# Kernel optimization log

Measured on AMD Instinct MI355X. Metric: run time of the kernel, lower is better.

## Reference

```python
import jax, jax.numpy as jnp
import numpy as np

NUM_RELATIONS = 65
NUM_GRAPHS = 1600


def rgcn_conv(x, src, dst, etype, W, Wroot, b):
    """PyG RGCNConv: per-relation mean aggregation + root transform + bias.
    out_i = x_i @ Wroot + b + sum_r mean_{j in N_r(i)} (x_j) @ W_r
    (mean-then-transform == transform-then-mean since W_r is linear).
    """
    N = x.shape[0]
    x_src = x[src]  # [E, in]
    etype_f = etype

    def body(acc, rW):
        r, Wr = rW
        m = (etype_f == r).astype(x.dtype)[:, None]  # [E,1]
        s = jax.ops.segment_sum(x_src * m, dst, num_segments=N)   # [N,in]
        cnt = jax.ops.segment_sum(m, dst, num_segments=N)          # [N,1]
        mean = s / jnp.maximum(cnt, 1.0)
        return acc + mean @ Wr, None

    acc0 = x @ Wroot + b
    out, _ = jax.lax.scan(body, acc0, (jnp.arange(W.shape[0]), W))
    return out


def setup_inputs() -> dict:
    key = jax.random.key(0)
    ks = jax.random.split(key, 20)
    N, E, F, H, M = 50000, 200000, 128, 256, 64
    x = jax.random.normal(ks[0], (N, F), dtype=jnp.float32)
    edge_index = jax.random.randint(ks[1], (2, E), 0, N, dtype=jnp.int64)
    edge_type = jax.random.randint(ks[2], (E,), 0, NUM_RELATIONS, dtype=jnp.int64)
    batch = jnp.sort(jax.random.randint(ks[3], (N,), 0, NUM_GRAPHS, dtype=jnp.int64))

    def glorot(k, shape):
        fan_in = shape[-2] if len(shape) > 1 else shape[-1]
        return jax.random.normal(k, shape, dtype=jnp.float32) / np.sqrt(fan_in)

    W1 = glorot(ks[4], (NUM_RELATIONS, F, H))
    root1 = glorot(ks[5], (F, H))
    b1 = jnp.zeros((H,), jnp.float32)
    W2 = glorot(ks[6], (NUM_RELATIONS, H, H))
    root2 = glorot(ks[7], (H, H))
    b2 = jnp.zeros((H,), jnp.float32)
    ws_w = glorot(ks[8], (H, 1))
    ws_b = jnp.zeros((1,), jnp.float32)
    m1w = glorot(ks[9], (H, M)); m1b = jnp.zeros((M,), jnp.float32)
    m2w = glorot(ks[10], (M, M)); m2b = jnp.zeros((M,), jnp.float32)
    m3w = glorot(ks[11], (M, M)); m3b = jnp.zeros((M,), jnp.float32)
    ow = glorot(ks[12], (M, 1)); ob = jnp.zeros((1,), jnp.float32)
    return {"x": x, "edge_index": edge_index, "edge_type": edge_type, "batch": batch,
            "W1": W1, "root1": root1, "b1": b1, "W2": W2, "root2": root2, "b2": b2,
            "ws_w": ws_w, "ws_b": ws_b, "m1w": m1w, "m1b": m1b, "m2w": m2w,
            "m2b": m2b, "m3w": m3w, "m3b": m3b, "ow": ow, "ob": ob}


def reference(x, edge_index, edge_type, batch, W1, root1, b1, W2, root2, b2,
              ws_w, ws_b, m1w, m1b, m2w, m2b, m3w, m3b, ow, ob):
    N = x.shape[0]
    # add_self_loops(fill_value=0): append self edges with relation 0
    loop = jnp.arange(N, dtype=edge_index.dtype)
    src = jnp.concatenate([edge_index[0], loop])
    dst = jnp.concatenate([edge_index[1], loop])
    et = jnp.concatenate([edge_type, jnp.zeros((N,), edge_type.dtype)])

    h = jax.nn.relu(rgcn_conv(x, src, dst, et, W1, root1, b1))   # dropout: eval
    h = jax.nn.relu(rgcn_conv(h, src, dst, et, W2, root2, b2))

    # WeightedSum pooling
    w = jax.nn.sigmoid(h @ ws_w + ws_b)                          # [N,1]
    emb = jax.ops.segment_sum(w * h, batch, num_segments=NUM_GRAPHS)  # [G,H]

    # MLP (3 layers; eval batch-norm with default stats ~ identity)
    z = jax.nn.relu(emb @ m1w + m1b)
    z = jax.nn.relu(z @ m2w + m2b)
    z = z @ m3w + m3b
    return z @ ow + ob
```

## Files before the change

### kernel.cpp

```cpp
#include <hip/hip_runtime.h>
#include <math.h>

#define N_NODES 50000
#define E_REAL  200000
#define E_MEAN  250000
#define NREL    65
#define HDIM    256
#define NGRAPH  1600
#define NB_R    ((E_REAL + 255) / 256)
#define NB_CNT  ((E_MEAN + 255) / 256)
#define TOT_HIST (NREL * NB_R)
#define MB      64
#define MAX_PB  3264
#define GRID_I  ((N_NODES + MB - 1) / MB)

typedef __attribute__((ext_vector_type(8))) short short8;
typedef __attribute__((ext_vector_type(4))) float floatx4;
typedef const __attribute__((address_space(1))) void GPtr;
typedef __attribute__((address_space(3))) void LPtr;

__device__ __forceinline__ unsigned short f2bf(float f) {
    unsigned int u = __float_as_uint(f);
    unsigned int r = u + 0x7FFFu + ((u >> 16) & 1u);
    return (unsigned short)(r >> 16);
}
__device__ __forceinline__ float bf2f(unsigned short u) {
    return __uint_as_float(((unsigned int)u) << 16);
}

__device__ __forceinline__ void gl_lds16(const unsigned short* g, unsigned short* l) {
    __builtin_amdgcn_global_load_lds((GPtr*)g,
        (LPtr*)(unsigned int)(unsigned long long)(void*)l, 16, 0, 0);
}

__global__ void count_kernel(const int* __restrict__ src, const int* __restrict__ dst,
                             const int* __restrict__ et, int* __restrict__ cnt,
                             int* __restrict__ blockHist, int* __restrict__ cntD) {
    __shared__ int lhist[NREL];
    int t = threadIdx.x;
    if (t < NREL) lhist[t] = 0;
    __syncthreads();
    int e = blockIdx.x * 256 + t;
    if (e < E_REAL) {
        int d = dst[e], r = et[e];
        atomicAdd(&cnt[d * NREL + r], 1);
        atomicAdd(&cntD[d], 1);
        atomicAdd(&lhist[r], 1);
    } else if (e < E_MEAN) {
        atomicAdd(&cnt[(e - E_REAL) * NREL], 1);
    }
    __syncthreads();
    if (t < NREL && blockIdx.x < NB_R) blockHist[t * NB_R + blockIdx.x] = lhist[t];
}

__global__ void scan_part(const int* __restrict__ in, int* __restrict__ psum, int n) {
    __shared__ int red[1024];
    int t = threadIdx.x;
    int g = blockIdx.x * 1024 + t;
    red[t] = (g < n) ? in[g] : 0;
    __syncthreads();
    for (int off = 512; off >= 1; off >>= 1) {
        if (t < off) red[t] += red[t + off];
        __syncthreads();
    }
    if (t == 0) psum[blockIdx.x] = red[0];
}

__global__ void scan_apply(const int* __restrict__ in, const int* __restrict__ psum,
                           int* __restrict__ out, int* __restrict__ out2, int n) {
    __shared__ int sums[1024];
    __shared__ int soff;
    int t = threadIdx.x;
    int b = blockIdx.x;
    int g = b * 1024 + t;
    if (t < 64) {
        int v = (t < b) ? psum[t] : 0;
        for (int off = 32; off >= 1; off >>= 1) v += __shfl_down(v, off, 64);
        if (t == 0) soff = v;
    }
    int v = (g < n) ? in[g] : 0;
    sums[t] = v;
    __syncthreads();
    for (int off = 1; off < 1024; off <<= 1) {
        int u = (t >= off) ? sums[t - off] : 0;
        __syncthreads();
        sums[t] += u;
        __syncthreads();
    }
    if (g < n) {
        int excl = soff + sums[t] - v;
        out[g] = excl;
        if (out2) out2[g] = excl;
    }
}

__global__ void meta_kernel(const int* __restrict__ baseArr,
                            int* __restrict__ relStart, int* __restrict__ relTot,
                            int* __restrict__ pBlockStart, int* __restrict__ relOfBlock,
                            int* __restrict__ npb) {
    __shared__ int sStart[NREL + 1];
    __shared__ int sPB[NREL + 1];
    int t = threadIdx.x;
    if (t < NREL) sStart[t] = baseArr[t * NB_R];
    if (t == 0) sStart[NREL] = E_REAL;
    __syncthreads();
    if (t < NREL) {
        relStart[t] = sStart[t];
        relTot[t] = sStart[t + 1] - sStart[t];
    }
    if (t == 0) {
        int a2 = 0;
        for (int r = 0; r < NREL; ++r) {
            sPB[r] = a2;
            int tot = sStart[r + 1] - sStart[r];
            a2 += (tot + MB - 1) / MB;
        }
        sPB[NREL] = a2;
        npb[0] = a2;
    }
    __syncthreads();
    if (t < NREL) pBlockStart[t] = sPB[t];
    int NPB = sPB[NREL];
    for (int b = t; b < NPB; b += 1024) {
        int lo = 0, hi = NREL - 1;
        while (lo < hi) { int mid = (lo + hi + 1) >> 1; if (sPB[mid] <= b) lo = mid; else hi = mid - 1; }
        relOfBlock[b] = lo;
    }
}

__global__ void scatter_sorted(const int* __restrict__ src, const int* __restrict__ dst,
                               const int* __restrict__ et, const int* __restrict__ base,
                               int* __restrict__ perm, int* __restrict__ cursorD,
                               int* __restrict__ qofp) {
    __shared__ int lhist[NREL];
    int t = threadIdx.x;
    int b = blockIdx.x;
    if (t < NREL) lhist[t] = 0;
    __syncthreads();
    int e = b * 256 + t;
    if (e < E_REAL) {
        int d = dst[e], r = et[e];
        int local = atomicAdd(&lhist[r], 1);
        int p = base[r * NB_R + b] + local;
        perm[p] = e;
        int q = atomicAdd(&cursorD[d], 1);
        qofp[p] = q;
    }
}

__device__ __forceinline__ void cvt_row_chunk(const float* __restrict__ in,
                                              unsigned short* __restrict__ out,
                                              int i, int relu) {
    const float4* p = (const float4*)in + (size_t)i * 2;
    float4 a = p[0], b = p[1];
    float v[8] = {a.x, a.y, a.z, a.w, b.x, b.y, b.z, b.w};
    short8 o;
#pragma unroll
    for (int j = 0; j < 8; ++j) {
        float f = relu ? fmaxf(v[j], 0.f) : v[j];
        o[j] = (short)f2bf(f);
    }
    ((short8*)out)[i] = o;
}
__device__ __forceinline__ void cvt_wT_chunk(const float* __restrict__ W,
                                             unsigned short* __restrict__ out,
                                             int i, int K, int N) {
    int kc8 = K / 8;
    int kc = i % kc8;
    int tmp = i / kc8;
    int n = tmp % N;
    int r = tmp / N;
    const float* src = W + ((size_t)r * K + kc * 8) * N + n;
    short8 o;
#pragma unroll
    for (int j = 0; j < 8; ++j) o[j] = (short)f2bf(src[(size_t)j * N]);
    ((short8*)out)[i] = o;
}

__global__ void cvt_rows(const float* __restrict__ in, unsigned short* __restrict__ out,
                         int nchunk, int relu) {
    int i = blockIdx.x * 256 + threadIdx.x;
    if (i >= nchunk) return;
    cvt_row_chunk(in, out, i, relu);
}

#define CVT_NX  (N_NODES * 128 / 8)
#define CVT_W1  (NREL * 256 * 16)
#define CVT_W2  (NREL * 256 * 32)
#define CVT_R1  (256 * 16)
#define CVT_R2  (256 * 32)
#define CVT_TOT (CVT_NX + CVT_W1 + CVT_W2 + CVT_R1 + CVT_R2)
__global__ void cvt_all(const float* __restrict__ x, const float* __restrict__ W1,
                        const float* __restrict__ W2, const float* __restrict__ root1,
                        const float* __restrict__ root2,
                        unsigned short* __restrict__ xb, unsigned short* __restrict__ w1b,
                        unsigned short* __restrict__ w2b, unsigned short* __restrict__ r1b,
                        unsigned short* __restrict__ r2b) {
    int i = blockIdx.x * 256 + threadIdx.x;
    if (i < CVT_NX) { cvt_row_chunk(x, xb, i, 0); return; }
    i -= CVT_NX;
    if (i < CVT_W1) { cvt_wT_chunk(W1, w1b, i, 128, 256); return; }
    i -= CVT_W1;
    if (i < CVT_W2) { cvt_wT_chunk(W2, w2b, i, 256, 256); return; }
    i -= CVT_W2;
    if (i < CVT_R1) { cvt_wT_chunk(root1, r1b, i, 128, 256); return; }
    i -= CVT_R1;
    if (i < CVT_R2) { cvt_wT_chunk(root2, r2b, i, 256, 256); return; }
}

template<int K>
__device__ __forceinline__ void gemm_pass(const unsigned short* __restrict__ Bp,
                                          const unsigned short* lds,
                                          int lrow, int lk, floatx4 (&acc)[4][4]) {
    constexpr int KS = K / 32;
    short8 bb[3][4];
#pragma unroll
    for (int nf = 0; nf < 4; ++nf)
        bb[0][nf] = *(const short8*)(Bp + (size_t)(nf * 16 + lrow) * K + lk * 8);
#pragma unroll
    for (int nf = 0; nf < 4; ++nf)
        bb[1][nf] = *(const short8*)(Bp + (size_t)(nf * 16 + lrow) * K + 32 + lk * 8);
#pragma unroll
    for (int ks = 0; ks < KS; ++ks) {
        short8 a[4];
#pragma unroll
        for (int mf = 0; mf < 4; ++mf) {
            int row = mf * 16 + lrow;
            int c = (ks * 4 + lk) ^ (row & 7);
            a[mf] = *(const short8*)((const char*)lds + row * (K * 2) + c * 16);
        }
        if (ks + 2 < KS) {
#pragma unroll
            for (int nf = 0; nf < 4; ++nf)
                bb[(ks + 2) % 3][nf] = *(const short8*)(Bp + (size_t)(nf * 16 + lrow) * K + (ks + 2) * 32 + lk * 8);
        }
#pragma unroll
        for (int mf = 0; mf < 4; ++mf)
#pragma unroll
            for (int nf = 0; nf < 4; ++nf)
                acc[mf][nf] = __builtin_amdgcn_mfma_f32_16x16x32_bf16(a[mf], bb[ks % 3][nf], acc[mf][nf], 0, 0, 0);
    }
}

template<int K, bool EDGE>
__device__ __forceinline__ void stage_A(const unsigned short* __restrict__ A,
                                        unsigned short* lds, const int* ssrc,
                                        int rowbase, int t) {
    constexpr int CH = K / 8;
#pragma unroll
    for (int i = 0; i < (MB * CH) / 256; ++i) {
        int q = i * 256 + t;
        int row = q / CH, sl = q % CH;
        int srow;
        if constexpr (EDGE) srow = ssrc[row];
        else { srow = rowbase + row; if (srow >= N_NODES) srow = N_NODES - 1; }
        int cg = sl ^ (row & 7);
        gl_lds16(A + (size_t)srow * K + cg * 8, lds + q * 8);
    }
}

template<int K>
__global__ __launch_bounds__(256) void edge_msg(
    const unsigned short* __restrict__ A,
    const unsigned short* __restrict__ B,
    unsigned short* __restrict__ outB,
    const int* __restrict__ perm, const int* __restrict__ srcA,
    const int* __restrict__ dstA, const int* __restrict__ cnt,
    const int* __restrict__ relOfBlock, const int* __restrict__ pBlockStart,
    const int* __restrict__ relStart, const int* __restrict__ relTot,
    const int* __restrict__ npb, const int* __restrict__ qofp)
{
    __shared__ __align__(16) unsigned short lds[MB * HDIM];
    __shared__ int ssrc[MB];
    __shared__ int sqd[MB];
    __shared__ float sw[MB];
    int t = threadIdx.x;
    int b = blockIdx.x;
    if (b >= npb[0]) return;
    int rel = relOfBlock[b];
    int jb = b - pBlockStart[rel];
    int rs = relStart[rel];
    int nval = relTot[rel] - jb * MB; if (nval > MB) nval = MB;
    if (t < MB) {
        int s = 0, qd = 0; float w = 0.f;
        if (t < nval) {
            int p = rs + jb * MB + t;
            int e = perm[p];
            s = srcA[e];
            int d = dstA[e];
            w = 1.0f / (float)cnt[d * NREL + rel];
            qd = qofp[p];
        }
        ssrc[t] = s; sqd[t] = qd; sw[t] = w;
    }
    __syncthreads();
    stage_A<K, true>(A, lds, ssrc, 0, t);
    __syncthreads();

    int wave = t >> 6, lane = t & 63;
    int n0 = wave * 64;
    int lrow = lane & 15, lk = lane >> 4;
    floatx4 acc[4][4];
#pragma unroll
    for (int mf = 0; mf < 4; ++mf)
#pragma unroll
        for (int nf = 0; nf < 4; ++nf) acc[mf][nf] = (floatx4)0.f;
    gemm_pass<K>(B + ((size_t)rel * HDIM + n0) * K, lds, lrow, lk, acc);

    __syncthreads();
#pragma unroll
    for (int mf = 0; mf < 4; ++mf) {
        int mbase = mf * 16 + lk * 4;
#pragma unroll
        for (int i = 0; i < 4; ++i) {
            int row = mbase + i;
            float w = sw[row];
#pragma unroll
            for (int nf = 0; nf < 4; ++nf)
                lds[row * HDIM + n0 + nf * 16 + lrow] = f2bf(acc[mf][nf][i] * w);
        }
    }
    __syncthreads();
    for (int q = t; q < nval * 32; q += 256) {
        int row = q >> 5, c = q & 31;
        *(uint4*)(outB + (size_t)sqd[row] * HDIM + c * 8) = *(const uint4*)(lds + row * HDIM + c * 8);
    }
}

template<int K>
__global__ __launch_bounds__(256) void init_gemm(
    const unsigned short* __restrict__ A,
    const unsigned short* __restrict__ Broot,
    const unsigned short* __restrict__ Bself,
    const float* __restrict__ bias,
    unsigned short* __restrict__ outB,
    const int* __restrict__ cnt)
{
    __shared__ __align__(16) unsigned short lds[MB * HDIM];
    __shared__ float sw[MB];
    int t = threadIdx.x;
    int rowbase = blockIdx.x * MB;
    if (t < MB) {
        int srow = rowbase + t; if (srow >= N_NODES) srow = N_NODES - 1;
        sw[t] = 1.0f / (float)cnt[srow * NREL];
    }
    stage_A<K, false>(A, lds, nullptr, rowbase, t);
    __syncthreads();

    int wave = t >> 6, lane = t & 63;
    int n0 = wave * 64;
    int lrow = lane & 15, lk = lane >> 4;
    floatx4 acc[4][4];
#pragma unroll
    for (int mf = 0; mf < 4; ++mf)
#pragma unroll
        for (int nf = 0; nf < 4; ++nf) acc[mf][nf] = (floatx4)0.f;
    gemm_pass<K>(Bself + (size_t)n0 * K, lds, lrow, lk, acc);
#pragma unroll
    for (int mf = 0; mf < 4; ++mf) {
        int mbase = mf * 16 + lk * 4;
#pragma unroll
        for (int i = 0; i < 4; ++i) {
            float w = sw[mbase + i];
#pragma unroll
            for (int nf = 0; nf < 4; ++nf) acc[mf][nf][i] *= w;
        }
    }
    gemm_pass<K>(Broot + (size_t)n0 * K, lds, lrow, lk, acc);

    float bv[4];
#pragma unroll
    for (int nf = 0; nf < 4; ++nf) bv[nf] = bias[n0 + nf * 16 + lrow];
    __syncthreads();
#pragma unroll
    for (int mf = 0; mf < 4; ++mf) {
        int mbase = mf * 16 + lk * 4;
#pragma unroll
        for (int i = 0; i < 4; ++i) {
            int row = mbase + i;
#pragma unroll
            for (int nf = 0; nf < 4; ++nf)
                lds[row * HDIM + n0 + nf * 16 + lrow] = f2bf(acc[mf][nf][i] + bv[nf]);
        }
    }
    __syncthreads();
    int limit = N_NODES - rowbase; if (limit > MB) limit = MB;
    for (int q = t; q < limit * 32; q += 256) {
        int row = q >> 5, c = q & 31;
        *(uint4*)(outB + ((size_t)rowbase + row) * HDIM + c * 8) = *(const uint4*)(lds + row * HDIM + c * 8);
    }
}

template<int K, int MODE>
__global__ __launch_bounds__(256) void mfma_gemm(
    const unsigned short* __restrict__ A,
    const unsigned short* __restrict__ B,
    const unsigned short* __restrict__ Bself,
    const float* __restrict__ bias,
    float* __restrict__ outF,
    const int* __restrict__ perm, const int* __restrict__ srcA,
    const int* __restrict__ dstA, const int* __restrict__ cnt,
    const int* __restrict__ relOfBlock, const int* __restrict__ pBlockStart,
    const int* __restrict__ relStart, const int* __restrict__ relTot,
    const int* __restrict__ npb)
{
    constexpr bool EDGE = (MODE == 1);
    __shared__ __align__(16) unsigned short lds[MB * HDIM];
    __shared__ int ssrc[MB];
    __shared__ int sdst[MB];
    __shared__ float sw[MB];
    int t = threadIdx.x;
    int b = blockIdx.x;
    int rel = 0, rowbase = 0, jb = 0, rs = 0, nval = MB;
    if constexpr (EDGE) {
        if (b >= npb[0]) return;
        rel = relOfBlock[b];
        jb = b - pBlockStart[rel];
        rs = relStart[rel];
        nval = relTot[rel] - jb * MB; if (nval > MB) nval = MB;
        if (t < MB) {
            int s = 0, d = 0; float w = 0.f;
            if (t < nval) {
                int p = rs + jb * MB + t;
                int e = perm[p];
                s = srcA[e]; d = dstA[e];
                w = 1.0f / (float)cnt[d * NREL + rel];
            }
            ssrc[t] = s; sdst[t] = d; sw[t] = w;
        }
        __syncthreads();
    } else {
        rowbase = b * MB;
        if (t < MB) {
            int srow = rowbase + t; if (srow >= N_NODES) srow = N_NODES - 1;
            sw[t] = 1.0f / (float)cnt[srow * NREL];
        }
    }
    stage_A<K, EDGE>(A, lds, ssrc, rowbase, t);
    __syncthreads();

    int wave = t >> 6, lane = t & 63;
    int n0 = wave * 64;
    int lrow = lane & 15;
    int lk = lane >> 4;
    floatx4 acc[4][4];
#pragma unroll
    for (int mf = 0; mf < 4; ++mf)
#pragma unroll
        for (int nf = 0; nf < 4; ++nf) acc[mf][nf] = (floatx4)0.f;

    if constexpr (EDGE) {
        gemm_pass<K>(B + ((size_t)rel * HDIM + n0) * K, lds, lrow, lk, acc);
    } else {
        gemm_pass<K>(Bself + (size_t)n0 * K, lds, lrow, lk, acc);
#pragma unroll
        for (int mf = 0; mf < 4; ++mf) {
            int mbase = mf * 16 + lk * 4;
#pragma unroll
            for (int i = 0; i < 4; ++i) {
                float w = sw[mbase + i];
#pragma unroll
                for (int nf = 0; nf < 4; ++nf) acc[mf][nf][i] *= w;
            }
        }
        gemm_pass<K>(B + (size_t)n0 * K, lds, lrow, lk, acc);
    }

    if constexpr (MODE == 1) {
#pragma unroll
        for (int mf = 0; mf < 4; ++mf) {
            int mbase = mf * 16 + lk * 4;
#pragma unroll
            for (int i = 0; i < 4; ++i) {
                int mm = mbase + i;
                float w = sw[mm];
                if (w != 0.f) {
                    int drow = sdst[mm];
#pragma unroll
                    for (int nf = 0; nf < 4; ++nf) {
                        int col = n0 + nf * 16 + lrow;
                        atomicAdd(&outF[(size_t)drow * HDIM + col], acc[mf][nf][i] * w);
                    }
                }
            }
        }
    } else {
        float bv[4];
#pragma unroll
        for (int nf = 0; nf < 4; ++nf) bv[nf] = bias[n0 + nf * 16 + lrow];
#pragma unroll
        for (int mf = 0; mf < 4; ++mf) {
            int mbase = mf * 16 + lk * 4;
#pragma unroll
            for (int i = 0; i < 4; ++i) {
                int mm = rowbase + mbase + i;
                if (mm < N_NODES) {
#pragma unroll
                    for (int nf = 0; nf < 4; ++nf) {
                        int col = n0 + nf * 16 + lrow;
                        outF[(size_t)mm * HDIM + col] = acc[mf][nf][i] + bv[nf];
                    }
                }
            }
        }
    }
}

__global__ __launch_bounds__(256) void reduce_kernel(
    const unsigned short* __restrict__ hinit, const unsigned short* __restrict__ msg,
    const int* __restrict__ startD, const int* __restrict__ cntD,
    unsigned short* __restrict__ hout)
{
    int t = threadIdx.x;
    int lane = t & 63;
    int d = blockIdx.x * 4 + (t >> 6);
    if (d >= N_NODES) return;
    int s0 = startD[d], n = cntD[d];
    ushort4 hv = *(const ushort4*)(hinit + (size_t)d * HDIM + lane * 4);
    float v0 = bf2f(hv.x), v1 = bf2f(hv.y), v2 = bf2f(hv.z), v3 = bf2f(hv.w);
    const unsigned short* mp = msg + (size_t)s0 * HDIM + lane * 4;
#pragma unroll 4
    for (int q = 0; q < n; ++q) {
        ushort4 m = *(const ushort4*)(mp + (size_t)q * HDIM);
        v0 += bf2f(m.x); v1 += bf2f(m.y); v2 += bf2f(m.z); v3 += bf2f(m.w);
    }
    ushort4 o;
    o.x = f2bf(fmaxf(v0, 0.f)); o.y = f2bf(fmaxf(v1, 0.f));
    o.z = f2bf(fmaxf(v2, 0.f)); o.w = f2bf(fmaxf(v3, 0.f));
    *(ushort4*)(hout + (size_t)d * HDIM + lane * 4) = o;
}

__global__ __launch_bounds__(256) void pool_graph(
    const unsigned short* __restrict__ h, const int* __restrict__ batch,
    const float* __restrict__ wsw, const float* __restrict__ wsb,
    float* __restrict__ emb)
{
    int g = blockIdx.x;
    int t = threadIdx.x;
    __shared__ int slo, shi;
    __shared__ float sacc[4][HDIM];
    if (t == 0) {
        int lo = 0, hi = N_NODES;
        while (lo < hi) { int m = (lo + hi) >> 1; if (batch[m] < g) lo = m + 1; else hi = m; }
        slo = lo;
        int lo2 = lo, hi2 = N_NODES;
        while (lo2 < hi2) { int m = (lo2 + hi2) >> 1; if (batch[m] < g + 1) lo2 = m + 1; else hi2 = m; }
        shi = lo2;
    }
    __syncthreads();
    int wave = t >> 6, lane = t & 63;
    float4 wv = *(const float4*)(wsw + lane * 4);
    float wb = wsb[0];
    float a0 = 0.f, a1 = 0.f, a2 = 0.f, a3 = 0.f;
    for (int i = slo + wave; i < shi; i += 4) {
        ushort4 hv = *(const ushort4*)(h + (size_t)i * HDIM + lane * 4);
        float v0 = bf2f(hv.x), v1 = bf2f(hv.y), v2 = bf2f(hv.z), v3 = bf2f(hv.w);
        float pp = v0 * wv.x + v1 * wv.y + v2 * wv.z + v3 * wv.w;
        for (int off = 32; off >= 1; off >>= 1) pp += __shfl_down(pp, off, 64);
        float tot = __shfl(pp, 0, 64);
        float sig = 1.0f / (1.0f + expf(-(tot + wb)));
        a0 += sig * v0; a1 += sig * v1; a2 += sig * v2; a3 += sig * v3;
    }
    sacc[wave][lane * 4 + 0] = a0; sacc[wave][lane * 4 + 1] = a1;
    sacc[wave][lane * 4 + 2] = a2; sacc[wave][lane * 4 + 3] = a3;
    __syncthreads();
    emb[(size_t)g * HDIM + t] = sacc[0][t] + sacc[1][t] + sacc[2][t] + sacc[3][t];
}

__global__ void pool_kernel(const float* __restrict__ h, const int* __restrict__ batch,
                            const float* __restrict__ wsw, const float* __restrict__ wsb,
                            float* __restrict__ emb) {
    int i = blockIdx.x;
    int t = threadIdx.x;
    float v = fmaxf(h[(size_t)i * HDIM + t], 0.f);
    float p = v * wsw[t];
    for (int off = 32; off >= 1; off >>= 1) p += __shfl_down(p, off, 64);
    __shared__ float red[4];
    __shared__ float ssig;
    if ((t & 63) == 0) red[t >> 6] = p;
    __syncthreads();
    if (t == 0) {
        float s = red[0] + red[1] + red[2] + red[3] + wsb[0];
        ssig = 1.0f / (1.0f + expf(-s));
    }
    __syncthreads();
    atomicAdd(&emb[(size_t)batch[i] * HDIM + t], ssig * v);
}

__global__ void mlp_kernel(const float* __restrict__ emb,
                           const float* __restrict__ m1w, const float* __restrict__ m1b,
                           const float* __restrict__ m2w, const float* __restrict__ m2b,
                           const float* __restrict__ m3w, const float* __restrict__ m3b,
                           const float* __restrict__ ow,  const float* __restrict__ ob,
                           float* __restrict__ out) {
    int g = blockIdx.x;
    int t = threadIdx.x;
    __shared__ float e[HDIM];
    __shared__ float z1[64], z2[64];
    for (int idx = t; idx < HDIM; idx += 64) e[idx] = emb[(size_t)g * HDIM + idx];
    __syncthreads();
    float a = m1b[t];
    for (int k = 0; k < HDIM; ++k) a += e[k] * m1w[k * 64 + t];
    z1[t] = fmaxf(a, 0.f);
    __syncthreads();
    a = m2b[t];
    for (int k = 0; k < 64; ++k) a += z1[k] * m2w[k * 64 + t];
    z2[t] = fmaxf(a, 0.f);
    __syncthreads();
    a = m3b[t];
    for (int k = 0; k < 64; ++k) a += z2[k] * m3w[k * 64 + t];
    float p = a * ow[t];
    for (int off = 32; off >= 1; off >>= 1) p += __shfl_down(p, off, 64);
    if (t == 0) out[g] = p + ob[0];
}

extern "C" void kernel_launch(void* const* d_in, const int* in_sizes, int n_in,
                              void* d_out, int out_size, void* d_ws, size_t ws_size,
                              hipStream_t stream) {
    const float* x     = (const float*)d_in[0];
    const int*   ei    = (const int*)d_in[1];
    const int*   src   = ei;
    const int*   dst   = ei + E_REAL;
    const int*   et    = (const int*)d_in[2];
    const int*   batch = (const int*)d_in[3];
    const float* W1    = (const float*)d_in[4];
    const float* root1 = (const float*)d_in[5];
    const float* b1    = (const float*)d_in[6];
    const float* W2    = (const float*)d_in[7];
    const float* root2 = (const float*)d_in[8];
    const float* b2    = (const float*)d_in[9];
    const float* wsw   = (const float*)d_in[10];
    const float* wsb   = (const float*)d_in[11];
    const float* m1w   = (const float*)d_in[12];
    const float* m1b   = (const float*)d_in[13];
    const float* m2w   = (const float*)d_in[14];
    const float* m2b   = (const float*)d_in[15];
    const float* m3w   = (const float*)d_in[16];
    const float* m3b   = (const float*)d_in[17];
    const float* ow    = (const float*)d_in[18];
    const float* ob    = (const float*)d_in[19];

    char* ws = (char*)d_ws;
    size_t off = 0;
    auto alloc = [&](size_t bytes) {
        void* p = ws + off;
        off = (off + bytes + 255) & ~(size_t)255;
        return p;
    };
    int*   cnt       = (int*)alloc((size_t)N_NODES * NREL * 4);
    int*   blockHist = (int*)alloc((size_t)TOT_HIST * 4);
    int*   baseArr   = (int*)alloc((size_t)TOT_HIST * 4);
    int*   perm      = (int*)alloc((size_t)E_REAL * 4);
    int*   relStartA = (int*)alloc(NREL * 4);
    int*   relTotA   = (int*)alloc(NREL * 4);
    int*   pbStartA  = (int*)alloc(NREL * 4);
    int*   relOfBlk  = (int*)alloc(MAX_PB * 4);
    int*   npb       = (int*)alloc(4);
    int*   psumA     = (int*)alloc(64 * 4);
    int*   psumB     = (int*)alloc(64 * 4);
    unsigned short* xb  = (unsigned short*)alloc((size_t)N_NODES * 128 * 2);
    unsigned short* w1b = (unsigned short*)alloc((size_t)NREL * 256 * 128 * 2);
    unsigned short* w2b = (unsigned short*)alloc((size_t)NREL * 256 * 256 * 2);
    unsigned short* r1b = (unsigned short*)alloc((size_t)256 * 128 * 2);
    unsigned short* r2b = (unsigned short*)alloc((size_t)256 * 256 * 2);
    unsigned short* h1b = (unsigned short*)alloc((size_t)N_NODES * HDIM * 2);
    float* emb = (float*)alloc((size_t)NGRAPH * HDIM * 4);
    size_t off_common = off;

    unsigned short* hinit = (unsigned short*)alloc((size_t)N_NODES * HDIM * 2);
    unsigned short* msg   = (unsigned short*)alloc((size_t)E_REAL * HDIM * 2);
    int* qofp    = (int*)alloc((size_t)E_REAL * 4);
    int* cntD    = (int*)alloc((size_t)N_NODES * 4);
    int* startD  = (int*)alloc((size_t)N_NODES * 4);
    int* cursorD = (int*)alloc((size_t)N_NODES * 4);
    size_t need_fast = off;

    float* hf = nullptr;
    bool fast = (ws_size >= need_fast);
    if (!fast) {
        off = off_common;
        hf = (float*)alloc((size_t)N_NODES * HDIM * 4);
        char* hh = (char*)hf;
        qofp    = (int*)hh;                                 hh += (size_t)E_REAL * 4;
        cntD    = (int*)hh;                                 hh += (size_t)N_NODES * 4;
        startD  = (int*)hh;                                 hh += (size_t)N_NODES * 4;
        cursorD = (int*)hh;
        hinit = h1b;
        msg = h1b;
    }

    hipMemsetAsync(cnt, 0, (size_t)N_NODES * NREL * 4, stream);
    hipMemsetAsync(cntD, 0, (size_t)N_NODES * 4, stream);
    hipMemsetAsync(emb, 0, (size_t)NGRAPH * HDIM * 4, stream);

    count_kernel<<<NB_CNT, 256, 0, stream>>>(src, dst, et, cnt, blockHist, cntD);
    scan_part<<<64, 1024, 0, stream>>>(blockHist, psumA, TOT_HIST);
    scan_apply<<<64, 1024, 0, stream>>>(blockHist, psumA, baseArr, nullptr, TOT_HIST);
    meta_kernel<<<1, 1024, 0, stream>>>(baseArr, relStartA, relTotA, pbStartA, relOfBlk, npb);
    scan_part<<<64, 1024, 0, stream>>>(cntD, psumB, N_NODES);
    scan_apply<<<64, 1024, 0, stream>>>(cntD, psumB, startD, cursorD, N_NODES);
    scatter_sorted<<<NB_R, 256, 0, stream>>>(src, dst, et, baseArr, perm, cursorD, qofp);

    cvt_all<<<(CVT_TOT + 255) / 256, 256, 0, stream>>>(x, W1, W2, root1, root2,
                                                       xb, w1b, w2b, r1b, r2b);

    if (fast) {
        init_gemm<128><<<GRID_I, 256, 0, stream>>>(xb, r1b, w1b, b1, hinit, cnt);
        edge_msg<128><<<MAX_PB, 256, 0, stream>>>(xb, w1b, msg,
            perm, src, dst, cnt, relOfBlk, pbStartA, relStartA, relTotA, npb, qofp);
        reduce_kernel<<<N_NODES / 4, 256, 0, stream>>>(hinit, msg, startD, cntD, h1b);
        init_gemm<256><<<GRID_I, 256, 0, stream>>>(h1b, r2b, w2b, b2, hinit, cnt);
        edge_msg<256><<<MAX_PB, 256, 0, stream>>>(h1b, w2b, msg,
            perm, src, dst, cnt, relOfBlk, pbStartA, relStartA, relTotA, npb, qofp);
        reduce_kernel<<<N_NODES / 4, 256, 0, stream>>>(hinit, msg, startD, cntD, h1b);
        pool_graph<<<NGRAPH, 256, 0, stream>>>(h1b, batch, wsw, wsb, emb);
    } else {
        mfma_gemm<128, 0><<<GRID_I, 256, 0, stream>>>(xb, r1b, w1b, b1, hf,
            nullptr, nullptr, nullptr, cnt, nullptr, nullptr, nullptr, nullptr, nullptr);
        mfma_gemm<128, 1><<<MAX_PB, 256, 0, stream>>>(xb, w1b, nullptr, nullptr, hf,
            perm, src, dst, cnt, relOfBlk, pbStartA, relStartA, relTotA, npb);
        cvt_rows<<<(N_NODES * HDIM / 8 + 255) / 256, 256, 0, stream>>>(hf, h1b, N_NODES * HDIM / 8, 1);
        mfma_gemm<256, 0><<<GRID_I, 256, 0, stream>>>(h1b, r2b, w2b, b2, hf,
            nullptr, nullptr, nullptr, cnt, nullptr, nullptr, nullptr, nullptr, nullptr);
        mfma_gemm<256, 1><<<MAX_PB, 256, 0, stream>>>(h1b, w2b, nullptr, nullptr, hf,
            perm, src, dst, cnt, relOfBlk, pbStartA, relStartA, relTotA, npb);
        pool_kernel<<<N_NODES, 256, 0, stream>>>(hf, batch, wsw, wsb, emb);
    }
    mlp_kernel<<<NGRAPH, 64, 0, stream>>>(emb, m1w, m1b, m2w, m2b, m3w, m3b, ow, ob, (float*)d_out);
}
```

Baseline: 367.4 us.

## Fuse layer-2 reduce into pooling, merge scans, prefetch weights before barrier

Merges the two prefix-scan pairs into single launches that handle both arrays by block index. Fuses the second layer's per-node message reduction and ReLU directly into the graph pooling kernel, so the layer-2 activation is never written to memory and one launch plus one memset are dropped. In both GEMM kernels the first weight-fragment loads are issued before the LDS staging barrier, so their latency overlaps the A staging. The fused pool runs one block per graph, which gives less parallelism than the old per-node reduce and may load-balance poorly across graphs of different sizes.

Measured after the change: 345.0 us. 1.06x faster.

```diff
diff --git a/kernel.cpp b/kernel.cpp
--- a/kernel.cpp
+++ b/kernel.cpp
@@ -13,6 +13,8 @@
 #define MB      64
 #define MAX_PB  3264
 #define GRID_I  ((N_NODES + MB - 1) / MB)
+#define NSA     ((TOT_HIST + 1023) / 1024)
+#define NSB     ((N_NODES + 1023) / 1024)
 
 typedef __attribute__((ext_vector_type(8))) short short8;
 typedef __attribute__((ext_vector_type(4))) float floatx4;
@@ -53,31 +55,44 @@
     if (t < NREL && blockIdx.x < NB_R) blockHist[t * NB_R + blockIdx.x] = lhist[t];
 }
 
-__global__ void scan_part(const int* __restrict__ in, int* __restrict__ psum, int n) {
+__global__ void scan_part2(const int* __restrict__ inA, const int* __restrict__ inB,
+                           int* __restrict__ psumA, int* __restrict__ psumB) {
     __shared__ int red[1024];
     int t = threadIdx.x;
-    int g = blockIdx.x * 1024 + t;
+    int b = blockIdx.x;
+    const int* in; int n; int bi;
+    if (b < NSA) { in = inA; n = TOT_HIST; bi = b; }
+    else         { in = inB; n = N_NODES;  bi = b - NSA; }
+    int g = bi * 1024 + t;
     red[t] = (g < n) ? in[g] : 0;
     __syncthreads();
     for (int off = 512; off >= 1; off >>= 1) {
         if (t < off) red[t] += red[t + off];
         __syncthreads();
     }
-    if (t == 0) psum[blockIdx.x] = red[0];
-}
-
-__global__ void scan_apply(const int* __restrict__ in, const int* __restrict__ psum,
-                           int* __restrict__ out, int* __restrict__ out2, int n) {
+    if (t == 0) {
+        if (b < NSA) psumA[bi] = red[0];
+        else         psumB[bi] = red[0];
+    }
+}
+
+__global__ void scan_apply2(const int* __restrict__ inA, const int* __restrict__ inB,
+                            const int* __restrict__ psumA, const int* __restrict__ psumB,
+                            int* __restrict__ outA, int* __restrict__ outB,
+                            int* __restrict__ outB2) {
     __shared__ int sums[1024];
     __shared__ int soff;
     int t = threadIdx.x;
     int b = blockIdx.x;
-    int g = b * 1024 + t;
+    const int* in; const int* ps; int n; int bi;
+    if (b < NSA) { in = inA; ps = psumA; n = TOT_HIST; bi = b; }
+    else         { in = inB; ps = psumB; n = N_NODES;  bi = b - NSA; }
     if (t < 64) {
-        int v = (t < b) ? psum[t] : 0;
+        int v = (t < bi) ? ps[t] : 0;
         for (int off = 32; off >= 1; off >>= 1) v += __shfl_down(v, off, 64);
         if (t == 0) soff = v;
     }
+    int g = bi * 1024 + t;
     int v = (g < n) ? in[g] : 0;
     sums[t] = v;
     __syncthreads();
@@ -89,8 +104,8 @@
     }
     if (g < n) {
         int excl = soff + sums[t] - v;
-        out[g] = excl;
-        if (out2) out2[g] = excl;
+        if (b < NSA) outA[g] = excl;
+        else { outB[g] = excl; outB2[g] = excl; }
     }
 }
 
@@ -209,17 +224,27 @@
 }
 
 template<int K>
-__device__ __forceinline__ void gemm_pass(const unsigned short* __restrict__ Bp,
+__device__ __forceinline__ void ring_init(const unsigned short* __restrict__ Bp,
+                                          int lrow, int lk,
+                                          short8 (&b0)[4], short8 (&b1)[4]) {
+#pragma unroll
+    for (int nf = 0; nf < 4; ++nf)
+        b0[nf] = *(const short8*)(Bp + (size_t)(nf * 16 + lrow) * K + lk * 8);
+#pragma unroll
+    for (int nf = 0; nf < 4; ++nf)
+        b1[nf] = *(const short8*)(Bp + (size_t)(nf * 16 + lrow) * K + 32 + lk * 8);
+}
+
+template<int K>
+__device__ __forceinline__ void gemm_main(const unsigned short* __restrict__ Bp,
                                           const unsigned short* lds,
-                                          int lrow, int lk, floatx4 (&acc)[4][4]) {
+                                          int lrow, int lk,
+                                          short8 (&b0)[4], short8 (&b1)[4],
+                                          floatx4 (&acc)[4][4]) {
     constexpr int KS = K / 32;
     short8 bb[3][4];
 #pragma unroll
-    for (int nf = 0; nf < 4; ++nf)
-        bb[0][nf] = *(const short8*)(Bp + (size_t)(nf * 16 + lrow) * K + lk * 8);
-#pragma unroll
-    for (int nf = 0; nf < 4; ++nf)
-        bb[1][nf] = *(const short8*)(Bp + (size_t)(nf * 16 + lrow) * K + 32 + lk * 8);
+    for (int nf = 0; nf < 4; ++nf) { bb[0][nf] = b0[nf]; bb[1][nf] = b1[nf]; }
 #pragma unroll
     for (int ks = 0; ks < KS; ++ks) {
         short8 a[4];
@@ -240,6 +265,15 @@
             for (int nf = 0; nf < 4; ++nf)
                 acc[mf][nf] = __builtin_amdgcn_mfma_f32_16x16x32_bf16(a[mf], bb[ks % 3][nf], acc[mf][nf], 0, 0, 0);
     }
+}
+
+template<int K>
+__device__ __forceinline__ void gemm_pass(const unsigned short* __restrict__ Bp,
+                                          const unsigned short* lds,
+                                          int lrow, int lk, floatx4 (&acc)[4][4]) {
+    short8 b0[4], b1[4];
+    ring_init<K>(Bp, lrow, lk, b0, b1);
+    gemm_main<K>(Bp, lds, lrow, lk, b0, b1, acc);
 }
 
 template<int K, bool EDGE>
@@ -294,18 +328,23 @@
         ssrc[t] = s; sqd[t] = qd; sw[t] = w;
     }
     __syncthreads();
-    stage_A<K, true>(A, lds, ssrc, 0, t);
-    __syncthreads();
 
     int wave = t >> 6, lane = t & 63;
     int n0 = wave * 64;
     int lrow = lane & 15, lk = lane >> 4;
+    const unsigned short* Bp = B + ((size_t)rel * HDIM + n0) * K;
+
+    stage_A<K, true>(A, lds, ssrc, 0, t);
+    short8 b0[4], b1[4];
+    ring_init<K>(Bp, lrow, lk, b0, b1);
+    __syncthreads();
+
     floatx4 acc[4][4];
 #pragma unroll
     for (int mf = 0; mf < 4; ++mf)
 #pragma unroll
         for (int nf = 0; nf < 4; ++nf) acc[mf][nf] = (floatx4)0.f;
-    gemm_pass<K>(B + ((size_t)rel * HDIM + n0) * K, lds, lrow, lk, acc);
+    gemm_main<K>(Bp, lds, lrow, lk, b0, b1, acc);
 
     __syncthreads();
 #pragma unroll
@@ -344,18 +383,21 @@
         int srow = rowbase + t; if (srow >= N_NODES) srow = N_NODES - 1;
         sw[t] = 1.0f / (float)cnt[srow * NREL];
     }
-    stage_A<K, false>(A, lds, nullptr, rowbase, t);
-    __syncthreads();
-
     int wave = t >> 6, lane = t & 63;
     int n0 = wave * 64;
     int lrow = lane & 15, lk = lane >> 4;
+
+    stage_A<K, false>(A, lds, nullptr, rowbase, t);
+    short8 b0[4], b1[4];
+    ring_init<K>(Bself + (size_t)n0 * K, lrow, lk, b0, b1);
+    __syncthreads();
+
     floatx4 acc[4][4];
 #pragma unroll
     for (int mf = 0; mf < 4; ++mf)
 #pragma unroll
         for (int nf = 0; nf < 4; ++nf) acc[mf][nf] = (floatx4)0.f;
-    gemm_pass<K>(Bself + (size_t)n0 * K, lds, lrow, lk, acc);
+    gemm_main<K>(Bself + (size_t)n0 * K, lds, lrow, lk, b0, b1, acc);
 #pragma unroll
     for (int mf = 0; mf < 4; ++mf) {
         int mbase = mf * 16 + lk * 4;
@@ -530,10 +572,11 @@
     *(ushort4*)(hout + (size_t)d * HDIM + lane * 4) = o;
 }
 
-__global__ __launch_bounds__(256) void pool_graph(
-    const unsigned short* __restrict__ h, const int* __restrict__ batch,
-    const float* __restrict__ wsw, const float* __restrict__ wsb,
-    float* __restrict__ emb)
+__global__ __launch_bounds__(256) void reduce_pool(
+    const unsigned short* __restrict__ hinit, const unsigned short* __restrict__ msg,
+    const int* __restrict__ startD, const int* __restrict__ cntD,
+    const int* __restrict__ batch, const float* __restrict__ wsw,
+    const float* __restrict__ wsb, float* __restrict__ emb)
 {
     int g = blockIdx.x;
     int t = threadIdx.x;
@@ -552,9 +595,17 @@
     float4 wv = *(const float4*)(wsw + lane * 4);
     float wb = wsb[0];
     float a0 = 0.f, a1 = 0.f, a2 = 0.f, a3 = 0.f;
-    for (int i = slo + wave; i < shi; i += 4) {
-        ushort4 hv = *(const ushort4*)(h + (size_t)i * HDIM + lane * 4);
+    for (int d = slo + wave; d < shi; d += 4) {
+        int s0 = startD[d], n = cntD[d];
+        ushort4 hv = *(const ushort4*)(hinit + (size_t)d * HDIM + lane * 4);
         float v0 = bf2f(hv.x), v1 = bf2f(hv.y), v2 = bf2f(hv.z), v3 = bf2f(hv.w);
+        const unsigned short* mp = msg + (size_t)s0 * HDIM + lane * 4;
+        for (int q = 0; q < n; ++q) {
+            ushort4 m = *(const ushort4*)(mp + (size_t)q * HDIM);
+            v0 += bf2f(m.x); v1 += bf2f(m.y); v2 += bf2f(m.z); v3 += bf2f(m.w);
+        }
+        v0 = fmaxf(v0, 0.f); v1 = fmaxf(v1, 0.f);
+        v2 = fmaxf(v2, 0.f); v3 = fmaxf(v3, 0.f);
         float pp = v0 * wv.x + v1 * wv.y + v2 * wv.z + v3 * wv.w;
         for (int off = 32; off >= 1; off >>= 1) pp += __shfl_down(pp, off, 64);
         float tot = __shfl(pp, 0, 64);
@@ -691,14 +742,12 @@
 
     hipMemsetAsync(cnt, 0, (size_t)N_NODES * NREL * 4, stream);
     hipMemsetAsync(cntD, 0, (size_t)N_NODES * 4, stream);
-    hipMemsetAsync(emb, 0, (size_t)NGRAPH * HDIM * 4, stream);
 
     count_kernel<<<NB_CNT, 256, 0, stream>>>(src, dst, et, cnt, blockHist, cntD);
-    scan_part<<<64, 1024, 0, stream>>>(blockHist, psumA, TOT_HIST);
-    scan_apply<<<64, 1024, 0, stream>>>(blockHist, psumA, baseArr, nullptr, TOT_HIST);
+    scan_part2<<<NSA + NSB, 1024, 0, stream>>>(blockHist, cntD, psumA, psumB);
+    scan_apply2<<<NSA + NSB, 1024, 0, stream>>>(blockHist, cntD, psumA, psumB,
+                                                baseArr, startD, cursorD);
     meta_kernel<<<1, 1024, 0, stream>>>(baseArr, relStartA, relTotA, pbStartA, relOfBlk, npb);
-    scan_part<<<64, 1024, 0, stream>>>(cntD, psumB, N_NODES);
-    scan_apply<<<64, 1024, 0, stream>>>(cntD, psumB, startD, cursorD, N_NODES);
     scatter_sorted<<<NB_R, 256, 0, stream>>>(src, dst, et, baseArr, perm, cursorD, qofp);
 
     cvt_all<<<(CVT_TOT + 255) / 256, 256, 0, stream>>>(x, W1, W2, root1, root2,
@@ -712,9 +761,10 @@
         init_gemm<256><<<GRID_I, 256, 0, stream>>>(h1b, r2b, w2b, b2, hinit, cnt);
         edge_msg<256><<<MAX_PB, 256, 0, stream>>>(h1b, w2b, msg,
             perm, src, dst, cnt, relOfBlk, pbStartA, relStartA, relTotA, npb, qofp);
-        reduce_kernel<<<N_NODES / 4, 256, 0, stream>>>(hinit, msg, startD, cntD, h1b);
-        pool_graph<<<NGRAPH, 256, 0, stream>>>(h1b, batch, wsw, wsb, emb);
+        reduce_pool<<<NGRAPH, 256, 0, stream>>>(hinit, msg, startD, cntD,
+                                                batch, wsw, wsb, emb);
     } else {
+        hipMemsetAsync(emb, 0, (size_t)NGRAPH * HDIM * 4, stream);
         mfma_gemm<128, 0><<<GRID_I, 256, 0, stream>>>(xb, r1b, w1b, b1, hf,
             nullptr, nullptr, nullptr, cnt, nullptr, nullptr, nullptr, nullptr, nullptr);
         mfma_gemm<128, 1><<<MAX_PB, 256, 0, stream>>>(xb, w1b, nullptr, nullptr, hf,
```
